# Kernel optimization log

Hardware: AMD Instinct MI355X
Metric: run time of the kernel (lower is better)

The kernel has to match this reference:

```python
import jax, jax.numpy as jnp
import numpy as np

B = 16384
HIST_LEN, DYN_DIM, STAT_DIM, TIME_DIM = 24, 8, 3, 8
N_STATIONS, EMB_DIM = 120, 16
IN_DIM = HIST_LEN * DYN_DIM + STAT_DIM + TIME_DIM + EMB_DIM  # 219
HIDDEN, OUT = 64, 1
GRID, K = 5, 3
NUM_BASIS = GRID + K  # 8


def make_grid(in_dim):
    # uniform extended grid on [-1, 1], pykan-style: G + 2k + 1 knots per input
    h = 2.0 / GRID
    pts = jnp.arange(-K, GRID + K + 1, dtype=jnp.float32) * h - 1.0  # [G+2k+1]
    return jnp.broadcast_to(pts, (in_dim, pts.shape[0]))


def b_splines(x, grid_pts):
    # x: [B, I], grid_pts: [I, G+2k+1] -> bases [B, I, G+k] via Cox-de Boor
    g = grid_pts[None]              # [1, I, M]
    xe = x[..., None]               # [B, I, 1]
    b = ((xe >= g[..., :-1]) & (xe < g[..., 1:])).astype(x.dtype)
    for p in range(1, K + 1):
        b = ((xe - g[..., : -(p + 1)]) / (g[..., p:-1] - g[..., : -(p + 1)]) * b[..., :-1]
             + (g[..., p + 1:] - xe) / (g[..., p + 1:] - g[..., 1:-p]) * b[..., 1:])
    return b  # [B, I, G+k]


def kan_layer(x, w_base, coef, grid_pts):
    # base path (silu residual) + spline path
    y_base = jax.nn.silu(x) @ w_base                              # [B, O]
    y_spline = jnp.einsum('big,iog->bo', b_splines(x, grid_pts), coef)
    return y_base + y_spline


def setup_inputs() -> dict:
    key = jax.random.key(0)
    ks = jax.random.split(key, 9)
    hist = jax.random.normal(ks[0], (B, HIST_LEN, DYN_DIM), dtype=jnp.float32)
    static = jax.random.normal(ks[1], (B, STAT_DIM), dtype=jnp.float32)
    time_feats = jax.random.normal(ks[2], (B, TIME_DIM), dtype=jnp.float32)
    st_idx = jax.random.randint(ks[3], (B,), 0, N_STATIONS)
    emb_table = jax.random.normal(ks[4], (N_STATIONS, EMB_DIM), dtype=jnp.float32)
    s1 = 1.0 / np.sqrt(IN_DIM)
    s2 = 1.0 / np.sqrt(HIDDEN)
    w_base1 = jax.random.normal(ks[5], (IN_DIM, HIDDEN), dtype=jnp.float32) * s1
    coef1 = jax.random.normal(ks[6], (IN_DIM, HIDDEN, NUM_BASIS), dtype=jnp.float32) * (0.1 * s1)
    w_base2 = jax.random.normal(ks[7], (HIDDEN, OUT), dtype=jnp.float32) * s2
    coef2 = jax.random.normal(ks[8], (HIDDEN, OUT, NUM_BASIS), dtype=jnp.float32) * (0.1 * s2)
    return {"hist": hist, "static": static, "time_feats": time_feats, "st_idx": st_idx,
            "emb_table": emb_table, "w_base1": w_base1, "coef1": coef1,
            "w_base2": w_base2, "coef2": coef2}


def reference(hist, static, time_feats, st_idx, emb_table, w_base1, coef1, w_base2, coef2):
    grid1 = make_grid(IN_DIM)
    grid2 = make_grid(HIDDEN)
    hist_flat = hist.reshape(hist.shape[0], -1)          # [B, hist_len*dyn_dim]
    emb = emb_table[st_idx]                              # [B, emb_dim]
    x = jnp.concatenate([hist_flat, static, time_feats, emb], axis=1)  # [B, 219]
    h = kan_layer(x, w_base1, coef1, grid1)              # [B, 64]
    out = kan_layer(h, w_base2, coef2, grid2)            # [B, 1]
    return out.squeeze(-1)                               # [B]
```

## Files before the change

kernel.cpp:

```cpp
#include <hip/hip_runtime.h>


typedef _Float16 half8 __attribute__((ext_vector_type(8)));
typedef float floatx4 __attribute__((ext_vector_type(4)));

#define XR 233

__device__ __forceinline__ float silu_f(float x) {
    return x / (1.0f + __expf(-x));
}

__device__ __forceinline__ void bspline8_dense(float x, float f[8]) {
    float u  = (x + 2.2f) * 2.5f;
    float fj = floorf(u);
    float t  = u - fj;
    int   j  = (int)fj;
    bool valid = (u >= 0.0f) && (u < 11.0f);
    float t2 = t * t, t3 = t2 * t, omt = 1.0f - t;
    float b0 = omt * omt * omt * (1.0f / 6.0f);
    float b1 = (3.0f * t3 - 6.0f * t2 + 4.0f) * (1.0f / 6.0f);
    float b2 = (-3.0f * t3 + 3.0f * t2 + 3.0f * t + 1.0f) * (1.0f / 6.0f);
    float b3 = t3 * (1.0f / 6.0f);
    if (!valid) { b0 = b1 = b2 = b3 = 0.0f; }
    int base = j - 3;
#pragma unroll
    for (int g = 0; g < 8; ++g) {
        int m = g - base;
        float v = (m == 0) ? b0 : 0.0f;
        v = (m == 1) ? b1 : v;
        v = (m == 2) ? b2 : v;
        v = (m == 3) ? b3 : v;
        f[g] = v;
    }
}

__device__ __forceinline__ half8 bspline_frag(float x) {
    float u  = (x + 2.2f) * 2.5f;
    float fj = floorf(u);
    float t  = u - fj;
    int   j  = (int)fj;
    bool valid = (u >= 0.0f) && (u < 11.0f);
    float t2 = t * t, t3 = t2 * t, omt = 1.0f - t;
    float b0 = omt * omt * omt * (1.0f / 6.0f);
    float b1 = (3.0f * t3 - 6.0f * t2 + 4.0f) * (1.0f / 6.0f);
    float b2 = (-3.0f * t3 + 3.0f * t2 + 3.0f * t + 1.0f) * (1.0f / 6.0f);
    float b3 = t3 * (1.0f / 6.0f);
    union { _Float16 h[4]; unsigned long long q; } p;
    p.h[0] = (_Float16)b0; p.h[1] = (_Float16)b1;
    p.h[2] = (_Float16)b2; p.h[3] = (_Float16)b3;
    unsigned long long lo = valid ? p.q : 0ull;
    int jc = valid ? j : 3;
    int sh = (jc - 3) * 16;
    unsigned long long rlo, rhi;
    if (sh >= 0) {
        rlo = (sh < 64) ? (lo << sh) : 0ull;
        rhi = (sh == 0) ? 0ull
            : (sh < 64) ? (lo >> (64 - sh))
                        : (lo << (sh - 64));
    } else {
        rlo = lo >> (-sh);
        rhi = 0ull;
    }
    union { unsigned long long q[2]; half8 v; } r;
    r.q[0] = rlo; r.q[1] = rhi;
    return r.v;
}

__global__ __launch_bounds__(256) void build_w(
    const float* __restrict__ wb1, const float* __restrict__ cf1,
    _Float16* __restrict__ wcat)
{
    int flat = blockIdx.x * 256 + threadIdx.x;
    int lane = flat & 63;
    int nt   = (flat >> 6) & 3;
    int st   = flat >> 8;
    int kg   = lane >> 4;
    int n    = nt * 16 + (lane & 15);
    _Float16 v[8];
    if (st < 7) {
#pragma unroll
        for (int j = 0; j < 8; ++j) {
            int i = st * 32 + kg * 8 + j;
            v[j] = (_Float16)((i < 219) ? wb1[i * 64 + n] : 0.0f);
        }
    } else {
        int i = (st - 7) * 4 + kg;
#pragma unroll
        for (int j = 0; j < 8; ++j)
            v[j] = (_Float16)((i < 219) ? cf1[(i * 64 + n) * 8 + j] : 0.0f);
    }
    *(half8*)(wcat + (size_t)flat * 8) = *(half8*)v;
}

__global__ __launch_bounds__(256) void kan_mfma(
    const float* __restrict__ hist,
    const float* __restrict__ statf,
    const float* __restrict__ timef,
    const int*   __restrict__ st_idx,
    const float* __restrict__ emb,
    const _Float16* __restrict__ wcat,
    const float* __restrict__ wb2,
    const float* __restrict__ cf2,
    float* __restrict__ out)
{
    __shared__ union {
        float xb[32 * XR];
        struct { float h[2][32 * 65]; float part[8 * 32]; } ep;
    } sm;

    const int tid  = threadIdx.x;
    const int lane = tid & 63;
    const int w    = __builtin_amdgcn_readfirstlane(tid >> 6);
    const int mt   = w & 1;
    const int kh   = w >> 1;
    const int bx   = blockIdx.x;
    const int row  = lane & 15;
    const int kg   = lane >> 4;

    {
        const int s = tid >> 3, q4 = tid & 7;
        const int b = bx * 32 + s;
        const float4* h4 = (const float4*)hist;
#pragma unroll
        for (int f = 0; f < 6; ++f) {
            int i4 = q4 + 8 * f;
            float4 v = h4[b * 48 + i4];
            sm.xb[s * XR + i4 * 4 + 0] = v.x;
            sm.xb[s * XR + i4 * 4 + 1] = v.y;
            sm.xb[s * XR + i4 * 4 + 2] = v.z;
            sm.xb[s * XR + i4 * 4 + 3] = v.w;
        }
    }
#pragma unroll
    for (int f = 0; f < 4; ++f) {
        int flat = f * 256 + tid;
        int s  = flat >> 5;
        int ii = 192 + (flat & 31);
        int b  = bx * 32 + s;
        float v;
        if (ii < 195)      v = statf[b * 3 + (ii - 192)];
        else if (ii < 203) v = timef[b * 8 + (ii - 195)];
        else if (ii < 219) v = emb[st_idx[b] * 16 + (ii - 203)];
        else               v = 0.0f;
        sm.xb[s * XR + ii] = v;
    }
    __syncthreads();

    const float* xrow = &sm.xb[(mt * 16 + row) * XR];

    floatx4 acc[4];
#pragma unroll
    for (int nt = 0; nt < 4; ++nt) acc[nt] = (floatx4){0.f, 0.f, 0.f, 0.f};

    for (int st = kh; st < 7; st += 2) {
        const _Float16* wp = wcat + (size_t)(st * 4) * 512 + lane * 8;
        half8 bf0 = *(const half8*)(wp);
        half8 bf1 = *(const half8*)(wp + 512);
        half8 bf2 = *(const half8*)(wp + 1024);
        half8 bf3 = *(const half8*)(wp + 1536);
        const int i0 = st * 32 + kg * 8;
        half8 af;
#pragma unroll
        for (int jj = 0; jj < 8; ++jj)
            af[jj] = (_Float16)silu_f(xrow[i0 + jj]);
        acc[0] = __builtin_amdgcn_mfma_f32_16x16x32_f16(af, bf0, acc[0], 0, 0, 0);
        acc[1] = __builtin_amdgcn_mfma_f32_16x16x32_f16(af, bf1, acc[1], 0, 0, 0);
        acc[2] = __builtin_amdgcn_mfma_f32_16x16x32_f16(af, bf2, acc[2], 0, 0, 0);
        acc[3] = __builtin_amdgcn_mfma_f32_16x16x32_f16(af, bf3, acc[3], 0, 0, 0);
    }

    const int st0 = (kh == 1) ? 7 : 8;
#pragma unroll 2
    for (int st = st0; st < 63; st += 2) {
        const _Float16* wp = wcat + (size_t)(st * 4) * 512 + lane * 8;
        half8 bf0 = *(const half8*)(wp);
        half8 bf1 = *(const half8*)(wp + 512);
        half8 bf2 = *(const half8*)(wp + 1024);
        half8 bf3 = *(const half8*)(wp + 1536);
        float x = xrow[(st - 7) * 4 + kg];
        half8 af = bspline_frag(x);
        acc[0] = __builtin_amdgcn_mfma_f32_16x16x32_f16(af, bf0, acc[0], 0, 0, 0);
        acc[1] = __builtin_amdgcn_mfma_f32_16x16x32_f16(af, bf1, acc[1], 0, 0, 0);
        acc[2] = __builtin_amdgcn_mfma_f32_16x16x32_f16(af, bf2, acc[2], 0, 0, 0);
        acc[3] = __builtin_amdgcn_mfma_f32_16x16x32_f16(af, bf3, acc[3], 0, 0, 0);
    }

    __syncthreads();
#pragma unroll
    for (int nt = 0; nt < 4; ++nt) {
#pragma unroll
        for (int r = 0; r < 4; ++r) {
            const int rr = mt * 16 + kg * 4 + r;
            const int cc = nt * 16 + row;
            sm.ep.h[kh][rr * 65 + cc] = acc[nt][r];
        }
    }
    __syncthreads();

    {
        const int s  = tid & 31;
        const int og = tid >> 5;
        float psum = 0.0f;
#pragma unroll
        for (int oo = 0; oo < 8; ++oo) {
            const int o = og * 8 + oo;
            float h = sm.ep.h[0][s * 65 + o] + sm.ep.h[1][s * 65 + o];
            psum = fmaf(silu_f(h), wb2[o], psum);
            float f2[8];
            bspline8_dense(h, f2);
#pragma unroll
            for (int g = 0; g < 8; ++g)
                psum = fmaf(f2[g], cf2[o * 8 + g], psum);
        }
        sm.ep.part[og * 32 + s] = psum;
    }
    __syncthreads();
    if (tid < 32) {
        float r = 0.0f;
#pragma unroll
        for (int og = 0; og < 8; ++og) r += sm.ep.part[og * 32 + tid];
        out[bx * 32 + tid] = r;
    }
}

extern "C" void kernel_launch(void* const* d_in, const int* in_sizes, int n_in,
                              void* d_out, int out_size, void* d_ws, size_t ws_size,
                              hipStream_t stream) {
    const float* hist  = (const float*)d_in[0];
    const float* statf = (const float*)d_in[1];
    const float* timef = (const float*)d_in[2];
    const int*   stidx = (const int*)  d_in[3];
    const float* emb   = (const float*)d_in[4];
    const float* wb1   = (const float*)d_in[5];
    const float* cf1   = (const float*)d_in[6];
    const float* wb2   = (const float*)d_in[7];
    const float* cf2   = (const float*)d_in[8];
    float* out = (float*)d_out;

    _Float16* wcat = (_Float16*)d_ws;

    build_w<<<63, 256, 0, stream>>>(wb1, cf1, wcat);
    kan_mfma<<<512, 256, 0, stream>>>(hist, statf, timef, stidx, emb,
                                      wcat, wb2, cf2, out);
}
```

Baseline: 94.08 us.

## Double rows per block to reuse weight fragments and prefetch next weights

Each block now processes 64 samples instead of 32, and each wave computes two 16-row M tiles that share the same loaded weight fragments, halving global weight loads per sample. The spline loop also software-prefetches the next step's weight fragments into registers. The grid shrinks from 512 to 256 blocks, which is about one block per CU on MI355X, so there is less parallelism to hide latency. Register and LDS use also rise, with the LDS buffer roughly 60KB.

```diff
diff --git a/kernel.cpp b/kernel.cpp
--- a/kernel.cpp
+++ b/kernel.cpp
@@ -104,26 +104,26 @@
     float* __restrict__ out)
 {
     __shared__ union {
-        float xb[32 * XR];
-        struct { float h[2][32 * 65]; float part[8 * 32]; } ep;
+        float xb[64 * XR];
+        struct { float h[2][64 * 65]; float part[4 * 64]; } ep;
     } sm;
 
     const int tid  = threadIdx.x;
     const int lane = tid & 63;
     const int w    = __builtin_amdgcn_readfirstlane(tid >> 6);
-    const int mt   = w & 1;
+    const int mh   = w & 1;
     const int kh   = w >> 1;
     const int bx   = blockIdx.x;
     const int row  = lane & 15;
     const int kg   = lane >> 4;
 
     {
-        const int s = tid >> 3, q4 = tid & 7;
-        const int b = bx * 32 + s;
+        const int s = tid >> 2, q4 = tid & 3;
+        const int b = bx * 64 + s;
         const float4* h4 = (const float4*)hist;
 #pragma unroll
-        for (int f = 0; f < 6; ++f) {
-            int i4 = q4 + 8 * f;
+        for (int f = 0; f < 12; ++f) {
+            int i4 = q4 + 4 * f;
             float4 v = h4[b * 48 + i4];
             sm.xb[s * XR + i4 * 4 + 0] = v.x;
             sm.xb[s * XR + i4 * 4 + 1] = v.y;
@@ -132,11 +132,11 @@
         }
     }
 #pragma unroll
-    for (int f = 0; f < 4; ++f) {
+    for (int f = 0; f < 8; ++f) {
         int flat = f * 256 + tid;
         int s  = flat >> 5;
         int ii = 192 + (flat & 31);
-        int b  = bx * 32 + s;
+        int b  = bx * 64 + s;
         float v;
         if (ii < 195)      v = statf[b * 3 + (ii - 192)];
         else if (ii < 203) v = timef[b * 8 + (ii - 195)];
@@ -146,11 +146,14 @@
     }
     __syncthreads();
 
-    const float* xrow = &sm.xb[(mt * 16 + row) * XR];
-
-    floatx4 acc[4];
-#pragma unroll
-    for (int nt = 0; nt < 4; ++nt) acc[nt] = (floatx4){0.f, 0.f, 0.f, 0.f};
+    const float* xrow0 = &sm.xb[(mh * 32 + row) * XR];
+    const float* xrow1 = xrow0 + 16 * XR;
+
+    floatx4 acc[2][4];
+#pragma unroll
+    for (int m = 0; m < 2; ++m)
+#pragma unroll
+        for (int nt = 0; nt < 4; ++nt) acc[m][nt] = (floatx4){0.f, 0.f, 0.f, 0.f};
 
     for (int st = kh; st < 7; st += 2) {
         const _Float16* wp = wcat + (size_t)(st * 4) * 512 + lane * 8;
@@ -159,51 +162,75 @@
         half8 bf2 = *(const half8*)(wp + 1024);
         half8 bf3 = *(const half8*)(wp + 1536);
         const int i0 = st * 32 + kg * 8;
-        half8 af;
-#pragma unroll
-        for (int jj = 0; jj < 8; ++jj)
-            af[jj] = (_Float16)silu_f(xrow[i0 + jj]);
-        acc[0] = __builtin_amdgcn_mfma_f32_16x16x32_f16(af, bf0, acc[0], 0, 0, 0);
-        acc[1] = __builtin_amdgcn_mfma_f32_16x16x32_f16(af, bf1, acc[1], 0, 0, 0);
-        acc[2] = __builtin_amdgcn_mfma_f32_16x16x32_f16(af, bf2, acc[2], 0, 0, 0);
-        acc[3] = __builtin_amdgcn_mfma_f32_16x16x32_f16(af, bf3, acc[3], 0, 0, 0);
-    }
-
-    const int st0 = (kh == 1) ? 7 : 8;
-#pragma unroll 2
-    for (int st = st0; st < 63; st += 2) {
+        half8 a0, a1;
+#pragma unroll
+        for (int jj = 0; jj < 8; ++jj) {
+            a0[jj] = (_Float16)silu_f(xrow0[i0 + jj]);
+            a1[jj] = (_Float16)silu_f(xrow1[i0 + jj]);
+        }
+        acc[0][0] = __builtin_amdgcn_mfma_f32_16x16x32_f16(a0, bf0, acc[0][0], 0, 0, 0);
+        acc[0][1] = __builtin_amdgcn_mfma_f32_16x16x32_f16(a0, bf1, acc[0][1], 0, 0, 0);
+        acc[0][2] = __builtin_amdgcn_mfma_f32_16x16x32_f16(a0, bf2, acc[0][2], 0, 0, 0);
+        acc[0][3] = __builtin_amdgcn_mfma_f32_16x16x32_f16(a0, bf3, acc[0][3], 0, 0, 0);
+        acc[1][0] = __builtin_amdgcn_mfma_f32_16x16x32_f16(a1, bf0, acc[1][0], 0, 0, 0);
+        acc[1][1] = __builtin_amdgcn_mfma_f32_16x16x32_f16(a1, bf1, acc[1][1], 0, 0, 0);
+        acc[1][2] = __builtin_amdgcn_mfma_f32_16x16x32_f16(a1, bf2, acc[1][2], 0, 0, 0);
+        acc[1][3] = __builtin_amdgcn_mfma_f32_16x16x32_f16(a1, bf3, acc[1][3], 0, 0, 0);
+    }
+
+    {
+        int st = (kh == 1) ? 7 : 8;
         const _Float16* wp = wcat + (size_t)(st * 4) * 512 + lane * 8;
         half8 bf0 = *(const half8*)(wp);
         half8 bf1 = *(const half8*)(wp + 512);
         half8 bf2 = *(const half8*)(wp + 1024);
         half8 bf3 = *(const half8*)(wp + 1536);
-        float x = xrow[(st - 7) * 4 + kg];
-        half8 af = bspline_frag(x);
-        acc[0] = __builtin_amdgcn_mfma_f32_16x16x32_f16(af, bf0, acc[0], 0, 0, 0);
-        acc[1] = __builtin_amdgcn_mfma_f32_16x16x32_f16(af, bf1, acc[1], 0, 0, 0);
-        acc[2] = __builtin_amdgcn_mfma_f32_16x16x32_f16(af, bf2, acc[2], 0, 0, 0);
-        acc[3] = __builtin_amdgcn_mfma_f32_16x16x32_f16(af, bf3, acc[3], 0, 0, 0);
-    }
-
-    __syncthreads();
-#pragma unroll
-    for (int nt = 0; nt < 4; ++nt) {
-#pragma unroll
-        for (int r = 0; r < 4; ++r) {
-            const int rr = mt * 16 + kg * 4 + r;
-            const int cc = nt * 16 + row;
-            sm.ep.h[kh][rr * 65 + cc] = acc[nt][r];
+        for (; st < 63; st += 2) {
+            const int stn = (st + 2 < 63) ? st + 2 : st;
+            const _Float16* wn = wcat + (size_t)(stn * 4) * 512 + lane * 8;
+            half8 n0 = *(const half8*)(wn);
+            half8 n1 = *(const half8*)(wn + 512);
+            half8 n2 = *(const half8*)(wn + 1024);
+            half8 n3 = *(const half8*)(wn + 1536);
+            const int xo = (st - 7) * 4 + kg;
+            float x0 = xrow0[xo];
+            float x1 = xrow1[xo];
+            half8 a0 = bspline_frag(x0);
+            half8 a1 = bspline_frag(x1);
+            acc[0][0] = __builtin_amdgcn_mfma_f32_16x16x32_f16(a0, bf0, acc[0][0], 0, 0, 0);
+            acc[0][1] = __builtin_amdgcn_mfma_f32_16x16x32_f16(a0, bf1, acc[0][1], 0, 0, 0);
+            acc[0][2] = __builtin_amdgcn_mfma_f32_16x16x32_f16(a0, bf2, acc[0][2], 0, 0, 0);
+            acc[0][3] = __builtin_amdgcn_mfma_f32_16x16x32_f16(a0, bf3, acc[0][3], 0, 0, 0);
+            acc[1][0] = __builtin_amdgcn_mfma_f32_16x16x32_f16(a1, bf0, acc[1][0], 0, 0, 0);
+            acc[1][1] = __builtin_amdgcn_mfma_f32_16x16x32_f16(a1, bf1, acc[1][1], 0, 0, 0);
+            acc[1][2] = __builtin_amdgcn_mfma_f32_16x16x32_f16(a1, bf2, acc[1][2], 0, 0, 0);
+            acc[1][3] = __builtin_amdgcn_mfma_f32_16x16x32_f16(a1, bf3, acc[1][3], 0, 0, 0);
+            bf0 = n0; bf1 = n1; bf2 = n2; bf3 = n3;
+        }
+    }
+
+    __syncthreads();
+#pragma unroll
+    for (int m = 0; m < 2; ++m) {
+#pragma unroll
+        for (int nt = 0; nt < 4; ++nt) {
+#pragma unroll
+            for (int r = 0; r < 4; ++r) {
+                const int rr = mh * 32 + m * 16 + kg * 4 + r;
+                const int cc = nt * 16 + row;
+                sm.ep.h[kh][rr * 65 + cc] = acc[m][nt][r];
+            }
         }
     }
     __syncthreads();
 
     {
-        const int s  = tid & 31;
-        const int og = tid >> 5;
+        const int s  = tid & 63;
+        const int og = tid >> 6;
         float psum = 0.0f;
 #pragma unroll
-        for (int oo = 0; oo < 8; ++oo) {
-            const int o = og * 8 + oo;
+        for (int oo = 0; oo < 16; ++oo) {
+            const int o = og * 16 + oo;
             float h = sm.ep.h[0][s * 65 + o] + sm.ep.h[1][s * 65 + o];
             psum = fmaf(silu_f(h), wb2[o], psum);
             float f2[8];
@@ -212,15 +239,12 @@
             for (int g = 0; g < 8; ++g)
                 psum = fmaf(f2[g], cf2[o * 8 + g], psum);
         }
-        sm.ep.part[og * 32 + s] = psum;
-    }
-    __syncthreads();
-    if (tid < 32) {
-        float r = 0.0f;
-#pragma unroll
-        for (int og = 0; og < 8; ++og) r += sm.ep.part[og * 32 + tid];
-        out[bx * 32 + tid] = r;
-    }
+        sm.ep.part[og * 64 + s] = psum;
+    }
+    __syncthreads();
+    if (tid < 64)
+        out[bx * 64 + tid] = sm.ep.part[tid] + sm.ep.part[64 + tid] +
+                             sm.ep.part[128 + tid] + sm.ep.part[192 + tid];
 }
 
 extern "C" void kernel_launch(void* const* d_in, const int* in_sizes, int n_in,
@@ -240,6 +264,6 @@
     _Float16* wcat = (_Float16*)d_ws;
 
     build_w<<<63, 256, 0, stream>>>(wb1, cf1, wcat);
-    kan_mfma<<<512, 256, 0, stream>>>(hist, statf, timef, stidx, emb,
+    kan_mfma<<<256, 256, 0, stream>>>(hist, statf, timef, stidx, emb,
                                       wcat, wb2, cf2, out);
 }
```

New measurement: 100.4 us. 1.07x slower.

## Halve rows per block and split K four ways across waves

Applied to the files above, without the earlier changes.

Each block now handles 16 batch rows instead of 32, and the four waves split the K dimension four ways instead of doing a 2x2 M/K split. The grid doubles to 1024 blocks and the launch bounds request 4 blocks per CU. The goal is more parallelism across the CUs and higher occupancy, with less shared memory per block. In exchange every block reloads the full fp16 weight matrix for half as many rows, and the epilogue reduction now sums four partial tiles. The build kernel gains one extra zero-padded K step so the spline loop divides evenly by 4.

```diff
diff --git a/kernel.cpp b/kernel.cpp
--- a/kernel.cpp
+++ b/kernel.cpp
@@ -92,7 +92,7 @@
     *(half8*)(wcat + (size_t)flat * 8) = *(half8*)v;
 }
 
-__global__ __launch_bounds__(256) void kan_mfma(
+__global__ __launch_bounds__(256, 4) void kan_mfma(
     const float* __restrict__ hist,
     const float* __restrict__ statf,
     const float* __restrict__ timef,
@@ -104,26 +104,24 @@
     float* __restrict__ out)
 {
     __shared__ union {
-        float xb[32 * XR];
-        struct { float h[2][32 * 65]; float part[8 * 32]; } ep;
+        float xb[16 * XR];
+        struct { float h[4][16 * 65]; float part[16 * 16]; } ep;
     } sm;
 
     const int tid  = threadIdx.x;
     const int lane = tid & 63;
-    const int w    = __builtin_amdgcn_readfirstlane(tid >> 6);
-    const int mt   = w & 1;
-    const int kh   = w >> 1;
+    const int q    = __builtin_amdgcn_readfirstlane(tid >> 6);
     const int bx   = blockIdx.x;
     const int row  = lane & 15;
     const int kg   = lane >> 4;
 
     {
-        const int s = tid >> 3, q4 = tid & 7;
-        const int b = bx * 32 + s;
+        const int s = tid >> 4, c = tid & 15;
+        const int b = bx * 16 + s;
         const float4* h4 = (const float4*)hist;
 #pragma unroll
-        for (int f = 0; f < 6; ++f) {
-            int i4 = q4 + 8 * f;
+        for (int f = 0; f < 3; ++f) {
+            int i4 = c + 16 * f;
             float4 v = h4[b * 48 + i4];
             sm.xb[s * XR + i4 * 4 + 0] = v.x;
             sm.xb[s * XR + i4 * 4 + 1] = v.y;
@@ -132,27 +130,27 @@
         }
     }
 #pragma unroll
-    for (int f = 0; f < 4; ++f) {
+    for (int f = 0; f < 3; ++f) {
         int flat = f * 256 + tid;
-        int s  = flat >> 5;
-        int ii = 192 + (flat & 31);
-        int b  = bx * 32 + s;
+        int s  = flat / 48;
+        int ii = 192 + (flat % 48);
+        int b  = bx * 16 + s;
         float v;
         if (ii < 195)      v = statf[b * 3 + (ii - 192)];
         else if (ii < 203) v = timef[b * 8 + (ii - 195)];
         else if (ii < 219) v = emb[st_idx[b] * 16 + (ii - 203)];
         else               v = 0.0f;
-        sm.xb[s * XR + ii] = v;
-    }
-    __syncthreads();
-
-    const float* xrow = &sm.xb[(mt * 16 + row) * XR];
+        if (ii < 233) sm.xb[s * XR + ii] = v;
+    }
+    __syncthreads();
+
+    const float* xrow = &sm.xb[row * XR];
 
     floatx4 acc[4];
 #pragma unroll
     for (int nt = 0; nt < 4; ++nt) acc[nt] = (floatx4){0.f, 0.f, 0.f, 0.f};
 
-    for (int st = kh; st < 7; st += 2) {
+    for (int st = q; st < 7; st += 4) {
         const _Float16* wp = wcat + (size_t)(st * 4) * 512 + lane * 8;
         half8 bf0 = *(const half8*)(wp);
         half8 bf1 = *(const half8*)(wp + 512);
@@ -169,20 +167,22 @@
         acc[3] = __builtin_amdgcn_mfma_f32_16x16x32_f16(af, bf3, acc[3], 0, 0, 0);
     }
 
-    const int st0 = (kh == 1) ? 7 : 8;
+    {
+        int st = 7 + ((q - 3) & 3);
 #pragma unroll 2
-    for (int st = st0; st < 63; st += 2) {
-        const _Float16* wp = wcat + (size_t)(st * 4) * 512 + lane * 8;
-        half8 bf0 = *(const half8*)(wp);
-        half8 bf1 = *(const half8*)(wp + 512);
-        half8 bf2 = *(const half8*)(wp + 1024);
-        half8 bf3 = *(const half8*)(wp + 1536);
-        float x = xrow[(st - 7) * 4 + kg];
-        half8 af = bspline_frag(x);
-        acc[0] = __builtin_amdgcn_mfma_f32_16x16x32_f16(af, bf0, acc[0], 0, 0, 0);
-        acc[1] = __builtin_amdgcn_mfma_f32_16x16x32_f16(af, bf1, acc[1], 0, 0, 0);
-        acc[2] = __builtin_amdgcn_mfma_f32_16x16x32_f16(af, bf2, acc[2], 0, 0, 0);
-        acc[3] = __builtin_amdgcn_mfma_f32_16x16x32_f16(af, bf3, acc[3], 0, 0, 0);
+        for (; st < 64; st += 4) {
+            const _Float16* wp = wcat + (size_t)(st * 4) * 512 + lane * 8;
+            half8 bf0 = *(const half8*)(wp);
+            half8 bf1 = *(const half8*)(wp + 512);
+            half8 bf2 = *(const half8*)(wp + 1024);
+            half8 bf3 = *(const half8*)(wp + 1536);
+            float x = xrow[(st - 7) * 4 + kg];
+            half8 af = bspline_frag(x);
+            acc[0] = __builtin_amdgcn_mfma_f32_16x16x32_f16(af, bf0, acc[0], 0, 0, 0);
+            acc[1] = __builtin_amdgcn_mfma_f32_16x16x32_f16(af, bf1, acc[1], 0, 0, 0);
+            acc[2] = __builtin_amdgcn_mfma_f32_16x16x32_f16(af, bf2, acc[2], 0, 0, 0);
+            acc[3] = __builtin_amdgcn_mfma_f32_16x16x32_f16(af, bf3, acc[3], 0, 0, 0);
+        }
     }
 
     __syncthreads();
@@ -190,21 +190,22 @@
     for (int nt = 0; nt < 4; ++nt) {
 #pragma unroll
         for (int r = 0; r < 4; ++r) {
-            const int rr = mt * 16 + kg * 4 + r;
+            const int rr = kg * 4 + r;
             const int cc = nt * 16 + row;
-            sm.ep.h[kh][rr * 65 + cc] = acc[nt][r];
+            sm.ep.h[q][rr * 65 + cc] = acc[nt][r];
         }
     }
     __syncthreads();
 
     {
-        const int s  = tid & 31;
-        const int og = tid >> 5;
+        const int s  = tid & 15;
+        const int og = tid >> 4;
         float psum = 0.0f;
 #pragma unroll
-        for (int oo = 0; oo < 8; ++oo) {
-            const int o = og * 8 + oo;
-            float h = sm.ep.h[0][s * 65 + o] + sm.ep.h[1][s * 65 + o];
+        for (int oo = 0; oo < 4; ++oo) {
+            const int o = og * 4 + oo;
+            float h = sm.ep.h[0][s * 65 + o] + sm.ep.h[1][s * 65 + o]
+                    + sm.ep.h[2][s * 65 + o] + sm.ep.h[3][s * 65 + o];
             psum = fmaf(silu_f(h), wb2[o], psum);
             float f2[8];
             bspline8_dense(h, f2);
@@ -212,14 +213,14 @@
             for (int g = 0; g < 8; ++g)
                 psum = fmaf(f2[g], cf2[o * 8 + g], psum);
         }
-        sm.ep.part[og * 32 + s] = psum;
-    }
-    __syncthreads();
-    if (tid < 32) {
+        sm.ep.part[og * 16 + s] = psum;
+    }
+    __syncthreads();
+    if (tid < 16) {
         float r = 0.0f;
 #pragma unroll
-        for (int og = 0; og < 8; ++og) r += sm.ep.part[og * 32 + tid];
-        out[bx * 32 + tid] = r;
+        for (int og = 0; og < 16; ++og) r += sm.ep.part[og * 16 + tid];
+        out[bx * 16 + tid] = r;
     }
 }
 
@@ -239,7 +240,7 @@
 
     _Float16* wcat = (_Float16*)d_ws;
 
-    build_w<<<63, 256, 0, stream>>>(wb1, cf1, wcat);
-    kan_mfma<<<512, 256, 0, stream>>>(hist, statf, timef, stidx, emb,
-                                      wcat, wb2, cf2, out);
-}
+    build_w<<<64, 256, 0, stream>>>(wb1, cf1, wcat);
+    kan_mfma<<<1024, 256, 0, stream>>>(hist, statf, timef, stidx, emb,
+                                       wcat, wb2, cf2, out);
+}
```

New measurement: 93.05 us. About the same (-1.1%).

## Stage weight tiles through double-buffered LDS shared across waves

Applied to the files above, without the earlier changes.

Before, each wave read its weight fragments straight from global memory (L2), and every wave pair loaded the same tiles. Now each of the four waves fetches one K-slab per chunk into registers and writes it to a double-buffered LDS stage, so the four waves share the global loads. The next chunk's load overlaps the MFMAs on the current one. This adds 16 block-wide barriers and extra LDS use (about 32KB more), which may lower occupancy. build_w now launches 64 blocks so a zero-padded 64th slab exists for the last chunk.

```diff
diff --git a/kernel.cpp b/kernel.cpp
--- a/kernel.cpp
+++ b/kernel.cpp
@@ -104,93 +104,110 @@
     float* __restrict__ out)
 {
     __shared__ union {
-        float xb[32 * XR];
+        struct {
+            float    xb[32 * XR];
+            _Float16 bst[2][4][2048];
+        } mn;
         struct { float h[2][32 * 65]; float part[8 * 32]; } ep;
     } sm;
 
     const int tid  = threadIdx.x;
     const int lane = tid & 63;
     const int w    = __builtin_amdgcn_readfirstlane(tid >> 6);
-    const int mt   = w & 1;
+    const int mh   = w & 1;
     const int kh   = w >> 1;
     const int bx   = blockIdx.x;
     const int row  = lane & 15;
     const int kg   = lane >> 4;
 
     {
-        const int s = tid >> 3, q4 = tid & 7;
+        const int s = tid >> 3, c8 = tid & 7;
         const int b = bx * 32 + s;
         const float4* h4 = (const float4*)hist;
 #pragma unroll
         for (int f = 0; f < 6; ++f) {
-            int i4 = q4 + 8 * f;
+            int i4 = c8 + 8 * f;
             float4 v = h4[b * 48 + i4];
-            sm.xb[s * XR + i4 * 4 + 0] = v.x;
-            sm.xb[s * XR + i4 * 4 + 1] = v.y;
-            sm.xb[s * XR + i4 * 4 + 2] = v.z;
-            sm.xb[s * XR + i4 * 4 + 3] = v.w;
-        }
-    }
-#pragma unroll
-    for (int f = 0; f < 4; ++f) {
+            sm.mn.xb[s * XR + i4 * 4 + 0] = v.x;
+            sm.mn.xb[s * XR + i4 * 4 + 1] = v.y;
+            sm.mn.xb[s * XR + i4 * 4 + 2] = v.z;
+            sm.mn.xb[s * XR + i4 * 4 + 3] = v.w;
+        }
+    }
+#pragma unroll
+    for (int f = 0; f < 6; ++f) {
         int flat = f * 256 + tid;
-        int s  = flat >> 5;
-        int ii = 192 + (flat & 31);
+        int s  = flat / 48;
+        int ii = 192 + (flat % 48);
         int b  = bx * 32 + s;
         float v;
         if (ii < 195)      v = statf[b * 3 + (ii - 192)];
         else if (ii < 203) v = timef[b * 8 + (ii - 195)];
         else if (ii < 219) v = emb[st_idx[b] * 16 + (ii - 203)];
         else               v = 0.0f;
-        sm.xb[s * XR + ii] = v;
+        if (ii < 233) sm.mn.xb[s * XR + ii] = v;
+    }
+
+    half8 rg[4];
+    {
+        const _Float16* src = wcat + (size_t)w * 2048 + lane * 8;
+#pragma unroll
+        for (int nt = 0; nt < 4; ++nt) rg[nt] = *(const half8*)(src + nt * 512);
+#pragma unroll
+        for (int nt = 0; nt < 4; ++nt)
+            *(half8*)&sm.mn.bst[0][w][nt * 512 + lane * 8] = rg[nt];
     }
     __syncthreads();
 
-    const float* xrow = &sm.xb[(mt * 16 + row) * XR];
+    const float* xrow = &sm.mn.xb[(mh * 16 + row) * XR];
 
     floatx4 acc[4];
 #pragma unroll
     for (int nt = 0; nt < 4; ++nt) acc[nt] = (floatx4){0.f, 0.f, 0.f, 0.f};
 
-    for (int st = kh; st < 7; st += 2) {
-        const _Float16* wp = wcat + (size_t)(st * 4) * 512 + lane * 8;
-        half8 bf0 = *(const half8*)(wp);
-        half8 bf1 = *(const half8*)(wp + 512);
-        half8 bf2 = *(const half8*)(wp + 1024);
-        half8 bf3 = *(const half8*)(wp + 1536);
-        const int i0 = st * 32 + kg * 8;
-        half8 af;
-#pragma unroll
-        for (int jj = 0; jj < 8; ++jj)
-            af[jj] = (_Float16)silu_f(xrow[i0 + jj]);
-        acc[0] = __builtin_amdgcn_mfma_f32_16x16x32_f16(af, bf0, acc[0], 0, 0, 0);
-        acc[1] = __builtin_amdgcn_mfma_f32_16x16x32_f16(af, bf1, acc[1], 0, 0, 0);
-        acc[2] = __builtin_amdgcn_mfma_f32_16x16x32_f16(af, bf2, acc[2], 0, 0, 0);
-        acc[3] = __builtin_amdgcn_mfma_f32_16x16x32_f16(af, bf3, acc[3], 0, 0, 0);
-    }
-
-    const int st0 = (kh == 1) ? 7 : 8;
-#pragma unroll 2
-    for (int st = st0; st < 63; st += 2) {
-        const _Float16* wp = wcat + (size_t)(st * 4) * 512 + lane * 8;
-        half8 bf0 = *(const half8*)(wp);
-        half8 bf1 = *(const half8*)(wp + 512);
-        half8 bf2 = *(const half8*)(wp + 1024);
-        half8 bf3 = *(const half8*)(wp + 1536);
-        float x = xrow[(st - 7) * 4 + kg];
-        half8 af = bspline_frag(x);
-        acc[0] = __builtin_amdgcn_mfma_f32_16x16x32_f16(af, bf0, acc[0], 0, 0, 0);
-        acc[1] = __builtin_amdgcn_mfma_f32_16x16x32_f16(af, bf1, acc[1], 0, 0, 0);
-        acc[2] = __builtin_amdgcn_mfma_f32_16x16x32_f16(af, bf2, acc[2], 0, 0, 0);
-        acc[3] = __builtin_amdgcn_mfma_f32_16x16x32_f16(af, bf3, acc[3], 0, 0, 0);
-    }
-
-    __syncthreads();
+    for (int c = 0; c < 16; ++c) {
+        const int buf = c & 1;
+        if (c < 15) {
+            const _Float16* src = wcat + (size_t)(4 * (c + 1) + w) * 2048 + lane * 8;
+#pragma unroll
+            for (int nt = 0; nt < 4; ++nt) rg[nt] = *(const half8*)(src + nt * 512);
+        }
+#pragma unroll
+        for (int u = 0; u < 2; ++u) {
+            const int sl = kh + 2 * u;
+            const int st = 4 * c + sl;
+            half8 af;
+            if (st < 7) {
+                const int i0 = st * 32 + kg * 8;
+#pragma unroll
+                for (int jj = 0; jj < 8; ++jj)
+                    af[jj] = (_Float16)silu_f(xrow[i0 + jj]);
+            } else {
+                af = bspline_frag(xrow[(st - 7) * 4 + kg]);
+            }
+            const _Float16* bp = &sm.mn.bst[buf][sl][lane * 8];
+            half8 b0 = *(const half8*)(bp);
+            half8 b1 = *(const half8*)(bp + 512);
+            half8 b2 = *(const half8*)(bp + 1024);
+            half8 b3 = *(const half8*)(bp + 1536);
+            acc[0] = __builtin_amdgcn_mfma_f32_16x16x32_f16(af, b0, acc[0], 0, 0, 0);
+            acc[1] = __builtin_amdgcn_mfma_f32_16x16x32_f16(af, b1, acc[1], 0, 0, 0);
+            acc[2] = __builtin_amdgcn_mfma_f32_16x16x32_f16(af, b2, acc[2], 0, 0, 0);
+            acc[3] = __builtin_amdgcn_mfma_f32_16x16x32_f16(af, b3, acc[3], 0, 0, 0);
+        }
+        if (c < 15) {
+#pragma unroll
+            for (int nt = 0; nt < 4; ++nt)
+                *(half8*)&sm.mn.bst[buf ^ 1][w][nt * 512 + lane * 8] = rg[nt];
+        }
+        __syncthreads();
+    }
+
 #pragma unroll
     for (int nt = 0; nt < 4; ++nt) {
 #pragma unroll
         for (int r = 0; r < 4; ++r) {
-            const int rr = mt * 16 + kg * 4 + r;
+            const int rr = mh * 16 + kg * 4 + r;
             const int cc = nt * 16 + row;
             sm.ep.h[kh][rr * 65 + cc] = acc[nt][r];
         }
@@ -239,7 +256,7 @@
 
     _Float16* wcat = (_Float16*)d_ws;
 
-    build_w<<<63, 256, 0, stream>>>(wb1, cf1, wcat);
+    build_w<<<64, 256, 0, stream>>>(wb1, cf1, wcat);
     kan_mfma<<<512, 256, 0, stream>>>(hist, statf, timef, stidx, emb,
                                       wcat, wb2, cf2, out);
 }
```

New measurement: 102.8 us. 9.2% more time.
